# Kernel tuning notes

Hardware: AMD Instinct MI355X
Metric: run time of the kernel (lower is better)

Reference implementation:

```python
import jax, jax.numpy as jnp
import numpy as np

B, N, L, H, K = 65536, 32, 8, 256, 8
RMIN, RMAX = -10.0, 10.0
MIN_BIN, MIN_SLOPE = 1e-4, 1e-4
P = 3 * K + 1  # params per feature per spline


def setup_inputs() -> dict:
    key = jax.random.key(0)
    ks = jax.random.split(key, 20)
    def rn(k, shape, s=0.05):
        return (jax.random.normal(k, shape, dtype=jnp.float32) * s)
    inp = {
        'x': jax.random.normal(ks[0], (B, N), dtype=jnp.float32),
        'sc_scale': 1.0 + rn(ks[1], (L, N)),
        'sc_shift': rn(ks[2], (L, N)),
        'W_in': rn(ks[3], (L, N, H)), 'b_in': rn(ks[4], (L, H)),
        'W1a': rn(ks[5], (L, H, H)), 'b1a': rn(ks[6], (L, H)),
        'W1b': rn(ks[7], (L, H, H)), 'b1b': rn(ks[8], (L, H)),
        'W2a': rn(ks[9], (L, H, H)), 'b2a': rn(ks[10], (L, H)),
        'W2b': rn(ks[11], (L, H, H)), 'b2b': rn(ks[12], (L, H)),
        'W_out': rn(ks[13], (L, H, N * P)), 'b_out': rn(ks[14], (L, N * P)),
        'perms': jnp.asarray(np.stack([np.random.RandomState(i).permutation(N) for i in range(L)]).astype(np.int32)),
    }
    return inp


def _conditioner(mx, Wi, bi, W1a, b1a, W1b, b1b, W2a, b2a, W2b, b2b, Wo, bo):
    # mx: [B, N] masked input -> [B, N, P] spline params
    h = mx @ Wi + bi
    r = jax.nn.relu(jax.nn.relu(h @ W1a + b1a) @ W1b + b1b)
    h = h + r
    r = jax.nn.relu(jax.nn.relu(h @ W2a + b2a) @ W2b + b2b)
    h = h + r
    h = jax.nn.relu(h)
    out = h @ Wo + bo
    return out.reshape(mx.shape[0], N, P)


def _rqs_forward(x, params):
    # x: [B, N]; params: [B, N, 3K+1]. distrax RationalQuadraticSpline forward.
    uw, uh, ud = params[..., :K], params[..., K:2 * K], params[..., 2 * K:]
    total = RMAX - RMIN
    w = jax.nn.softmax(uw, axis=-1) * (total - K * MIN_BIN) + MIN_BIN
    hgt = jax.nn.softmax(uh, axis=-1) * (total - K * MIN_BIN) + MIN_BIN
    zpad = jnp.zeros_like(w[..., :1])
    xp = RMIN + jnp.concatenate([zpad, jnp.cumsum(w, -1)], -1)   # [B,N,K+1]
    yp = RMIN + jnp.concatenate([zpad, jnp.cumsum(hgt, -1)], -1)
    offset = float(np.log(np.expm1(1.0 - MIN_SLOPE)))
    d = jax.nn.softplus(ud + offset) + MIN_SLOPE                  # [B,N,K+1]
    inside = (x > RMIN) & (x < RMAX)
    xc = jnp.clip(x, RMIN, RMAX)
    # per-element bin search (knot positions vary per element)
    idx = jnp.clip(jnp.sum((xc[..., None] >= xp).astype(jnp.int32), -1) - 1, 0, K - 1)
    g = lambda a, i: jnp.take_along_axis(a, i[..., None], -1)[..., 0]
    xk, xk1 = g(xp, idx), g(xp, idx + 1)
    yk, yk1 = g(yp, idx), g(yp, idx + 1)
    dk, dk1 = g(d, idx), g(d, idx + 1)
    bw = xk1 - xk
    bh = yk1 - yk
    s = bh / bw
    z = jnp.clip((xc - xk) / bw, 0.0, 1.0)
    zz = z * (1.0 - z)
    denom = s + (dk1 + dk - 2.0 * s) * zz
    y = yk + bh * (s * z * z + dk * zz) / denom
    ld = 2.0 * jnp.log(s) + jnp.log(dk1 * z * z + 2.0 * s * zz + dk * (1.0 - z) ** 2) - 2.0 * jnp.log(denom)
    return jnp.where(inside, y, x), jnp.where(inside, ld, 0.0)


def reference(x, sc_scale, sc_shift, W_in, b_in, W1a, b1a, W1b, b1b,
              W2a, b2a, W2b, b2b, W_out, b_out, perms):
    mask0 = (jnp.arange(N) % 2).astype(bool)  # True = identity (masked)
    logdet = jnp.zeros(x.shape[0], dtype=x.dtype)
    for i in range(L):
        # Permute
        x = x[:, perms[i]]
        # Scalar affine on all features (mask_all = all-False coupling)
        x = x * sc_scale[i] + sc_shift[i]
        logdet = logdet + jnp.sum(jnp.log(jnp.abs(sc_scale[i])))
        # RQ-spline masked coupling
        mask = mask0 if i % 2 == 0 else ~mask0
        mx = jnp.where(mask, x, 0.0)
        params = _conditioner(mx, W_in[i], b_in[i], W1a[i], b1a[i], W1b[i], b1b[i],
                              W2a[i], b2a[i], W2b[i], b2b[i], W_out[i], b_out[i])
        y, ld = _rqs_forward(x, params)
        x = jnp.where(mask, x, y)
        logdet = logdet + jnp.sum(jnp.where(mask, 0.0, ld), axis=-1)
    # standard-normal base log prob
    logp = -0.5 * jnp.sum(x * x, axis=-1) - 0.5 * N * float(np.log(2.0 * np.pi))
    return logp + logdet
```

## Files before the change

### kernel.cpp

```cpp
#include <hip/hip_runtime.h>
#include <hip/hip_bf16.h>

typedef __attribute__((ext_vector_type(8))) short bf16x8;
typedef __attribute__((ext_vector_type(16))) float f32x16;
typedef __attribute__((ext_vector_type(2))) float f32x2;

#define DEVFN __device__ __forceinline__

constexpr int NFEAT = 32, NLAYER = 8, HID = 256;
constexpr int HS  = 264;
constexpr int MXS = 40;
constexpr int XS  = 33;
constexpr int WIN_E  = 2 * 256 * 16;
constexpr int WH_E   = 16 * 256 * 16;
constexpr int WOUT_E = 16 * 512 * 16;
constexpr int LAYER_E = WIN_E + 4 * WH_E + WOUT_E;
constexpr size_t WT_BYTES = (size_t)LAYER_E * NLAYER * 2;
constexpr size_t WS_NEEDED = WT_BYTES + NLAYER * 512 * 4 + 4;

constexpr float MIN_BIN = 1e-4f, MIN_SLOPE = 1e-4f;
constexpr float SOFTPLUS_OFF = 0.5411666f;
constexpr float WSCALE = 20.0f - 8.0f * MIN_BIN;

DEVFN unsigned short bf16r(float f) {
    unsigned u = __float_as_uint(f);
    u += 0x7fffu + ((u >> 16) & 1u);
    return (unsigned short)(u >> 16);
}
#if defined(__gfx950__) && __has_builtin(__builtin_amdgcn_cvt_pk_bf16_f32)
DEVFN unsigned pack2(float a, float b) {
    auto r = __builtin_amdgcn_cvt_pk_bf16_f32(a, b);
    return __builtin_bit_cast(unsigned, r);
}
#else
DEVFN unsigned pack2(float a, float b) {
    return (unsigned)bf16r(a) | ((unsigned)bf16r(b) << 16);
}
#endif
DEVFN float bflo(unsigned v) { return __uint_as_float(v << 16); }
DEVFN float bfhi(unsigned v) { return __uint_as_float(v & 0xffff0000u); }
DEVFN float frcp(float x) { return __builtin_amdgcn_rcpf(x); }
DEVFN f32x2 vmax0(f32x2 v) {
// ... 38 lines not shown
            dst[o] = (short)bf16r(lb[kk * 256 + n]);
        }
    } else if (b < 656) {
        int id = b - 528; int l = id >> 4, ks = id & 15; int par = l & 1;
        const float* src = Wout + (size_t)l * 256 * 800 + ks * 16 * 800;
        for (int k = 0; k < 16; k++)
            for (int c = t; c < 800; c += 256) lb[k * 800 + c] = src[k * 800 + c];
        __syncthreads();
        short* dst = wt + (size_t)l * LAYER_E + WIN_E + 4 * WH_E + ks * 8192;
#pragma unroll
        for (int i = 0; i < 32; i++) {
            int o = t + i * 256; int c = o >> 4, kk = o & 15;
            int u = c >> 5, p = c & 31;
            float v = (p < 25) ? lb[kk * 800 + (2 * u + par) * 25 + p] : 0.0f;
            dst[o] = (short)bf16r(v);
        }
    } else {
#pragma unroll
        for (int i = 0; i < 16; i++) {
            int idx = t + i * 256;
            int l = idx >> 9, c = idx & 511, u = c >> 5, p = c & 31;
            bo_t[idx] = (p < 25) ? bout[l * 800 + (2 * u + (l & 1)) * 25 + p] : 0.0f;
        }
        lb[t] = logf(fabsf(scS[t]));
        __syncthreads();
        for (int s = 128; s > 0; s >>= 1) { if (t < s) lb[t] += lb[t + s]; __syncthreads(); }
        if (t == 0) *sld = lb[0];
    }
}

template<int KSTEPS, int NSUB, int DEPTH>
DEVFN void gemm_flip(const short* __restrict__ wt, int ntot, int nbase,
                     const unsigned short* __restrict__ B, int bs,
                     f32x16 (&acc)[NSUB][2])
{
    constexpr int D = (KSTEPS < DEPTH) ? KSTEPS : DEPTH;
    const int lane = threadIdx.x & 63;
    const int l31 = lane & 31, l5 = lane >> 5;
    const bf16x8* __restrict__ w8 = (const bf16x8*)wt;
    const int wb = (nbase + l31) * 2 + l5;
    const int krow = ntot * 2;
    bf16x8 a[D][NSUB];
#pragma unroll
    for (int p = 0; p < D; p++)
#pragma unroll
        for (int s = 0; s < NSUB; s++) a[p][s] = w8[(size_t)p * krow + wb + s * 64];
    const unsigned short* bp = B + l31 * bs + l5 * 8;
#pragma unroll
    for (int k = 0; k < KSTEPS; k++) {
        bf16x8 b0 = *(const bf16x8*)(bp + k * 16);
        bf16x8 b1 = *(const bf16x8*)(bp + 32 * bs + k * 16);
#pragma unroll
        for (int s = 0; s < NSUB; s++) {
            acc[s][0] = __builtin_amdgcn_mfma_f32_32x32x16_bf16(a[k % D][s], b0, acc[s][0], 0, 0, 0);
            acc[s][1] = __builtin_amdgcn_mfma_f32_32x32x16_bf16(a[k % D][s], b1, acc[s][1], 0, 0, 0);
        }
        if (k + D < KSTEPS) {
#pragma unroll
            for (int s = 0; s < NSUB; s++) a[k % D][s] = w8[(size_t)(k + D) * krow + wb + s * 64];
        }
    }
}

DEVFN void binit(f32x16& a, const float* __restrict__ bias)
{
    const int q = (threadIdx.x >> 5) & 1;
    const float* bp = bias + 4 * q;
#pragma unroll
    for (int g = 0; g < 4; g++) {
        float4 b = *(const float4*)(bp + 8 * g);
        a[4*g+0] = b.x; a[4*g+1] = b.y; a[4*g+2] = b.z; a[4*g+3] = b.w;
    }
}

template<int MODE>
DEVFN void store_h(const f32x16& v, unsigned short* buf, int m0, int n0)
{
    const int lane = threadIdx.x & 63;
    const int m = m0 + (lane & 31);
    const int q = lane >> 5;
    unsigned short* rowp = buf + m * HS + n0 + 4 * q;
#pragma unroll
    for (int g = 0; g < 4; g++) {
        f32x2 r0 = {v[4*g+0], v[4*g+1]};
        f32x2 r1 = {v[4*g+2], v[4*g+3]};
        if (MODE >= 1) { r0 = vmax0(r0); r1 = vmax0(r1); }
        unsigned short* dst = rowp + 8 * g;
        if (MODE >= 2) {
            uint2 old = *(const uint2*)dst;
            r0 += (f32x2){bflo(old.x), bfhi(old.x)};
            r1 += (f32x2){bflo(old.y), bfhi(old.y)};
            if (MODE == 3) { r0 = vmax0(r0); r1 = vmax0(r1); }
        }
        uint2 pk;
        pk.x = pack2(r0.x, r0.y);
        pk.y = pack2(r1.x, r1.y);
        *(uint2*)dst = pk;
    }
}

__global__ __launch_bounds__(256, 2) void flow_kernel(
    const float* __restrict__ x_in, const float* __restrict__ scS, const float* __restrict__ scB,
    const float* __restrict__ bin, const float* __restrict__ b1a, const float* __restrict__ b1b,
    const float* __restrict__ b2a, const float* __restrict__ b2b,
    const int* __restrict__ perms,
    const short* __restrict__ wt, const float* __restrict__ bo_t, const float* __restrict__ sld,
    float* __restrict__ out)
{
    __shared__ __align__(16) unsigned short hS[64 * HS];
    __shared__ __align__(16) unsigned short uS[64 * HS];
    __shared__ float xS[64 * XS];
    __shared__ float redS[256];

    const int tid = threadIdx.x;
    const int wave = tid >> 6;
    const int lane = tid & 63;
    const int q = lane >> 5;
    const size_t rowbase = (size_t)blockIdx.x * 64;
    unsigned short* tS  = uS;
    unsigned short* mxS = uS;

#pragma unroll
    for (int i = 0; i < 8; i++) {
        int g = tid + i * 256;
        xS[(g >> 5) * XS + (g & 31)] = x_in[rowbase * NFEAT + g];
    }
    float ld_acc = 0.0f;
    __syncthreads();

    const int nbase = wave * 64;

#pragma unroll 1
    for (int l = 0; l < NLAYER; l++) {
        const int par = l & 1;
        const short* wb = wt + (size_t)l * LAYER_E;

        {
            int j = tid & 31; int r0 = (tid >> 5) * 8;
            int pj = perms[l * 32 + j];
            float sc = scS[l * 32 + j], sh = scB[l * 32 + j];
            float vals[8];
#pragma unroll
            for (int r = 0; r < 8; r++) vals[r] = xS[(r0 + r) * XS + pj] * sc + sh;
            __syncthreads();
            int keep = ((j & 1) != par);
#pragma unroll
            for (int r = 0; r < 8; r++) {
                xS[(r0 + r) * XS + j] = vals[r];
                mxS[(r0 + r) * MXS + j] = keep ? bf16r(vals[r]) : (unsigned short)0;
            }
            __syncthreads();
        }
        {
            f32x16 acc[2][2];
            binit(acc[0][0], bin + l * 256 + nbase);      binit(acc[0][1], bin + l * 256 + nbase);
            binit(acc[1][0], bin + l * 256 + nbase + 32); binit(acc[1][1], bin + l * 256 + nbase + 32);
            gemm_flip<2, 2, 2>(wb, 256, nbase, mxS, MXS, acc);
#pragma unroll
            for (int s = 0; s < 2; s++) {
                store_h<0>(acc[s][0], hS, 0,  nbase + s * 32);
                store_h<0>(acc[s][1], hS, 32, nbase + s * 32);
            }
            __syncthreads();
        }
        {
            f32x16 acc[2][2];
            binit(acc[0][0], b1a + l * 256 + nbase);      binit(acc[0][1], b1a + l * 256 + nbase);
            binit(acc[1][0], b1a + l * 256 + nbase + 32); binit(acc[1][1], b1a + l * 256 + nbase + 32);
            gemm_flip<16, 2, 4>(wb + WIN_E, 256, nbase, hS, HS, acc);
#pragma unroll
            for (int s = 0; s < 2; s++) {
                store_h<1>(acc[s][0], tS, 0,  nbase + s * 32);
                store_h<1>(acc[s][1], tS, 32, nbase + s * 32);
            }
            __syncthreads();
        }
        {
            f32x16 acc[2][2];
            binit(acc[0][0], b1b + l * 256 + nbase);      binit(acc[0][1], b1b + l * 256 + nbase);
            binit(acc[1][0], b1b + l * 256 + nbase + 32); binit(acc[1][1], b1b + l * 256 + nbase + 32);
            gemm_flip<16, 2, 4>(wb + WIN_E + WH_E, 256, nbase, tS, HS, acc);
#pragma unroll
            for (int s = 0; s < 2; s++) {
                store_h<2>(acc[s][0], hS, 0,  nbase + s * 32);
                store_h<2>(acc[s][1], hS, 32, nbase + s * 32);
            }
            __syncthreads();
        }
        {
            f32x16 acc[2][2];
            binit(acc[0][0], b2a + l * 256 + nbase);      binit(acc[0][1], b2a + l * 256 + nbase);
            binit(acc[1][0], b2a + l * 256 + nbase + 32); binit(acc[1][1], b2a + l * 256 + nbase + 32);
            gemm_flip<16, 2, 4>(wb + WIN_E + 2 * WH_E, 256, nbase, hS, HS, acc);
#pragma unroll
            for (int s = 0; s < 2; s++) {
                store_h<1>(acc[s][0], tS, 0,  nbase + s * 32);
                store_h<1>(acc[s][1], tS, 32, nbase + s * 32);
            }
            __syncthreads();
        }
        {
            f32x16 acc[2][2];
            binit(acc[0][0], b2b + l * 256 + nbase);      binit(acc[0][1], b2b + l * 256 + nbase);
            binit(acc[1][0], b2b + l * 256 + nbase + 32); binit(acc[1][1], b2b + l * 256 + nbase + 32);
            gemm_flip<16, 2, 4>(wb + WIN_E + 3 * WH_E, 256, nbase, tS, HS, acc);
#pragma unroll
            for (int s = 0; s < 2; s++) {
                store_h<3>(acc[s][0], hS, 0,  nbase + s * 32);
                store_h<3>(acc[s][1], hS, 32, nbase + s * 32);
            }
            __syncthreads();
        }
        {
            const short* wo = wb + WIN_E + 4 * WH_E;
            f32x16 acc[4][2];
            const float* bb = bo_t + l * 512 + wave * 128;
#pragma unroll
            for (int s = 0; s < 4; s++) { binit(acc[s][0], bb + s * 32); binit(acc[s][1], bb + s * 32); }
            gemm_flip<16, 4, 2>(wo, 512, wave * 128, hS, HS, acc);

#pragma unroll
            for (int s = 0; s < 4; s++) {
                float exch[16];
#pragma unroll
                for (int i = 0; i < 16; i++) {
                    float snd = q ? acc[s][0][i] : acc[s][1][i];
                    exch[i] = __shfl_xor(snd, 32, 64);
                }
                float A0[16], A1[16];
#pragma unroll
                for (int i = 0; i < 16; i++) {
                    float kept = q ? acc[s][1][i] : acc[s][0][i];
                    A0[i] = q ? exch[i] : kept;
                    A1[i] = q ? kept : exch[i];
                }
                float P[25];
#pragma unroll
                for (int p = 0; p < 25; p++) {
                    int rg = (p & 3) + 4 * (p >> 3);
                    P[p] = ((p >> 2) & 1) ? A1[rg] : A0[rg];
                }
                int n = 2 * (4 * wave + s) + par;
                float xv = xS[lane * XS + n];
                float ew[8], eh[8], sw = 0.f, sh2 = 0.f;
#pragma unroll
                for (int i = 0; i < 8; i++) { ew[i] = __expf(P[i]); sw += ew[i]; }
#pragma unroll
                for (int i = 0; i < 8; i++) { eh[i] = __expf(P[8 + i]); sh2 += eh[i]; }
                float fw = WSCALE * frcp(sw), fh = WSCALE * frcp(sh2);
                float w[8], hh[8];
#pragma unroll
                for (int i = 0; i < 8; i++) { w[i] = fmaf(ew[i], fw, MIN_BIN); hh[i] = fmaf(eh[i], fh, MIN_BIN); }

                bool inside = (xv > -10.0f) && (xv < 10.0f);
                float xc = fminf(fmaxf(xv, -10.0f), 10.0f);
                float cx = -10.0f + w[0], cy = -10.0f + hh[0];
                float xk = -10.0f, yk = -10.0f, bw = w[0], bh = hh[0];
                float udk = P[16], udk1 = P[17];
#pragma unroll
                for (int i = 1; i < 8; i++) {
                    bool take = (xc >= cx);
                    if (take) { xk = cx; yk = cy; bw = w[i]; bh = hh[i]; udk = P[16 + i]; udk1 = P[17 + i]; }
                    cx += w[i]; cy += hh[i];
                }
                float dk  = __logf(1.f + __expf(udk  + SOFTPLUS_OFF)) + MIN_SLOPE;
                float dk1 = __logf(1.f + __expf(udk1 + SOFTPLUS_OFF)) + MIN_SLOPE;
                float ibw = frcp(bw);
                float s_ = bh * ibw;
                float z = fminf(fmaxf((xc - xk) * ibw, 0.0f), 1.0f);
                float omz = 1.0f - z;
                float zz = z * omz;
                float denom = fmaf(dk1 + dk - 2.0f * s_, zz, s_);
                float idenom = frcp(denom);
                float y = fmaf(bh * fmaf(s_ * z, z, dk * zz), idenom, yk);
                float num = fmaf(dk1 * z, z, fmaf(2.0f * s_, zz, dk * omz * omz));
                float ldv = 2.0f * __logf(s_ * idenom) + __logf(num);
                xS[lane * XS + n] = inside ? y : xv;
                ld_acc += inside ? ldv : 0.0f;
            }
            __syncthreads();
        }
    }
    {
        int m = tid & 63, jg = tid >> 6;
        float s2 = 0.f;
#pragma unroll
        for (int j = 0; j < 8; j++) { float v = xS[m * XS + jg * 8 + j]; s2 += v * v; }
        redS[tid] = ld_acc - 0.5f * s2;
        __syncthreads();
        if (tid < 64) {
            float tot = redS[tid] + redS[tid + 64] + redS[tid + 128] + redS[tid + 192]
                      + *sld - 29.406033062549525f;
            out[rowbase + tid] = tot;
        }
    }
}

extern "C" void kernel_launch(void* const* d_in, const int* in_sizes, int n_in,
                              void* d_out, int out_size, void* d_ws, size_t ws_size,
                              hipStream_t stream) {
    if (ws_size < WS_NEEDED) return;
    const float* x    = (const float*)d_in[0];
    const float* scS  = (const float*)d_in[1];
    const float* scB  = (const float*)d_in[2];
    const float* Win  = (const float*)d_in[3];
    const float* bin  = (const float*)d_in[4];
    const float* W1a  = (const float*)d_in[5];
    const float* b1a  = (const float*)d_in[6];
    const float* W1b  = (const float*)d_in[7];
    const float* b1b  = (const float*)d_in[8];
    const float* W2a  = (const float*)d_in[9];
    const float* b2a  = (const float*)d_in[10];
    const float* W2b  = (const float*)d_in[11];
    const float* b2b  = (const float*)d_in[12];
    const float* Wout = (const float*)d_in[13];
    const float* bout = (const float*)d_in[14];
    const int* perms  = (const int*)d_in[15];

    short* wt   = (short*)d_ws;
    float* bo_t = (float*)((char*)d_ws + WT_BYTES);
    float* sld  = bo_t + NLAYER * 512;

    prep_kernel<<<657, 256, 0, stream>>>(Win, W1a, W1b, W2a, W2b, Wout, bout, scS, wt, bo_t, sld);
    flow_kernel<<<65536 / 64, 256, 0, stream>>>(x, scS, scB, bin, b1a, b1b, b2a, b2b,
                                                perms, wt, bo_t, sld, (float*)d_out);
}
```

Baseline: 573.9 us.

## Split each 64-row block across eight waves instead of four

Doubles the block to 512 threads so each wave computes 32 hidden columns (and 64 output columns) instead of 64/128. All GEMM stages, the spline epilogue, the x-permute stage and the final reduction are re-indexed for eight waves. The aim is more waves per CU and fewer accumulator registers per wave, which helps latency hiding. The cost is that each wave reuses every loaded activation fragment over fewer columns, so LDS reads per MFMA go up, and the barriers now cover more waves.

```diff
diff --git a/kernel.cpp b/kernel.cpp
--- a/kernel.cpp
+++ b/kernel.cpp
@@ -179,7 +179,7 @@
     }
 }
 
-__global__ __launch_bounds__(256, 2) void flow_kernel(
+__global__ __launch_bounds__(512, 4) void flow_kernel(
     const float* __restrict__ x_in, const float* __restrict__ scS, const float* __restrict__ scB,
     const float* __restrict__ bin, const float* __restrict__ b1a, const float* __restrict__ b1b,
     const float* __restrict__ b2a, const float* __restrict__ b2b,
@@ -190,7 +190,7 @@
     __shared__ __align__(16) unsigned short hS[64 * HS];
     __shared__ __align__(16) unsigned short uS[64 * HS];
     __shared__ float xS[64 * XS];
-    __shared__ float redS[256];
+    __shared__ float redS[512];
 
     const int tid = threadIdx.x;
     const int wave = tid >> 6;
@@ -201,14 +201,14 @@
     unsigned short* mxS = uS;
 
 #pragma unroll
-    for (int i = 0; i < 8; i++) {
-        int g = tid + i * 256;
+    for (int i = 0; i < 4; i++) {
+        int g = tid + i * 512;
         xS[(g >> 5) * XS + (g & 31)] = x_in[rowbase * NFEAT + g];
     }
     float ld_acc = 0.0f;
     __syncthreads();
 
-    const int nbase = wave * 64;
+    const int nbase = wave * 32;
 
 #pragma unroll 1
     for (int l = 0; l < NLAYER; l++) {
@@ -216,91 +216,76 @@
         const short* wb = wt + (size_t)l * LAYER_E;
 
         {
-            int j = tid & 31; int r0 = (tid >> 5) * 8;
+            int j = tid & 31; int r0 = (tid >> 5) * 4;
             int pj = perms[l * 32 + j];
             float sc = scS[l * 32 + j], sh = scB[l * 32 + j];
-            float vals[8];
-#pragma unroll
-            for (int r = 0; r < 8; r++) vals[r] = xS[(r0 + r) * XS + pj] * sc + sh;
+            float vals[4];
+#pragma unroll
+            for (int r = 0; r < 4; r++) vals[r] = xS[(r0 + r) * XS + pj] * sc + sh;
             __syncthreads();
             int keep = ((j & 1) != par);
 #pragma unroll
-            for (int r = 0; r < 8; r++) {
+            for (int r = 0; r < 4; r++) {
                 xS[(r0 + r) * XS + j] = vals[r];
                 mxS[(r0 + r) * MXS + j] = keep ? bf16r(vals[r]) : (unsigned short)0;
             }
             __syncthreads();
         }
         {
+            f32x16 acc[1][2];
+            binit(acc[0][0], bin + l * 256 + nbase);
+            binit(acc[0][1], bin + l * 256 + nbase);
+            gemm_flip<2, 1, 2>(wb, 256, nbase, mxS, MXS, acc);
+            store_h<0>(acc[0][0], hS, 0,  nbase);
+            store_h<0>(acc[0][1], hS, 32, nbase);
+            __syncthreads();
+        }
+        {
+            f32x16 acc[1][2];
+            binit(acc[0][0], b1a + l * 256 + nbase);
+            binit(acc[0][1], b1a + l * 256 + nbase);
+            gemm_flip<16, 1, 4>(wb + WIN_E, 256, nbase, hS, HS, acc);
+            store_h<1>(acc[0][0], tS, 0,  nbase);
+            store_h<1>(acc[0][1], tS, 32, nbase);
+            __syncthreads();
+        }
+        {
+            f32x16 acc[1][2];
+            binit(acc[0][0], b1b + l * 256 + nbase);
+            binit(acc[0][1], b1b + l * 256 + nbase);
+            gemm_flip<16, 1, 4>(wb + WIN_E + WH_E, 256, nbase, tS, HS, acc);
+            store_h<2>(acc[0][0], hS, 0,  nbase);
+            store_h<2>(acc[0][1], hS, 32, nbase);
+            __syncthreads();
+        }
+        {
+            f32x16 acc[1][2];
+            binit(acc[0][0], b2a + l * 256 + nbase);
+            binit(acc[0][1], b2a + l * 256 + nbase);
+            gemm_flip<16, 1, 4>(wb + WIN_E + 2 * WH_E, 256, nbase, hS, HS, acc);
+            store_h<1>(acc[0][0], tS, 0,  nbase);
+            store_h<1>(acc[0][1], tS, 32, nbase);
+            __syncthreads();
+        }
+        {
+            f32x16 acc[1][2];
+            binit(acc[0][0], b2b + l * 256 + nbase);
+            binit(acc[0][1], b2b + l * 256 + nbase);
+            gemm_flip<16, 1, 4>(wb + WIN_E + 3 * WH_E, 256, nbase, tS, HS, acc);
+            store_h<3>(acc[0][0], hS, 0,  nbase);
+            store_h<3>(acc[0][1], hS, 32, nbase);
+            __syncthreads();
+        }
+        {
+            const short* wo = wb + WIN_E + 4 * WH_E;
             f32x16 acc[2][2];
-            binit(acc[0][0], bin + l * 256 + nbase);      binit(acc[0][1], bin + l * 256 + nbase);
-            binit(acc[1][0], bin + l * 256 + nbase + 32); binit(acc[1][1], bin + l * 256 + nbase + 32);
-            gemm_flip<2, 2, 2>(wb, 256, nbase, mxS, MXS, acc);
+            const float* bb = bo_t + l * 512 + wave * 64;
+#pragma unroll
+            for (int s = 0; s < 2; s++) { binit(acc[s][0], bb + s * 32); binit(acc[s][1], bb + s * 32); }
+            gemm_flip<16, 2, 2>(wo, 512, wave * 64, hS, HS, acc);
+
 #pragma unroll
             for (int s = 0; s < 2; s++) {
-                store_h<0>(acc[s][0], hS, 0,  nbase + s * 32);
-                store_h<0>(acc[s][1], hS, 32, nbase + s * 32);
-            }
-            __syncthreads();
-        }
-        {
-            f32x16 acc[2][2];
-            binit(acc[0][0], b1a + l * 256 + nbase);      binit(acc[0][1], b1a + l * 256 + nbase);
-            binit(acc[1][0], b1a + l * 256 + nbase + 32); binit(acc[1][1], b1a + l * 256 + nbase + 32);
-            gemm_flip<16, 2, 4>(wb + WIN_E, 256, nbase, hS, HS, acc);
-#pragma unroll
-            for (int s = 0; s < 2; s++) {
-                store_h<1>(acc[s][0], tS, 0,  nbase + s * 32);
-                store_h<1>(acc[s][1], tS, 32, nbase + s * 32);
-            }
-            __syncthreads();
-        }
-        {
-            f32x16 acc[2][2];
-            binit(acc[0][0], b1b + l * 256 + nbase);      binit(acc[0][1], b1b + l * 256 + nbase);
-            binit(acc[1][0], b1b + l * 256 + nbase + 32); binit(acc[1][1], b1b + l * 256 + nbase + 32);
-            gemm_flip<16, 2, 4>(wb + WIN_E + WH_E, 256, nbase, tS, HS, acc);
-#pragma unroll
-            for (int s = 0; s < 2; s++) {
-                store_h<2>(acc[s][0], hS, 0,  nbase + s * 32);
-                store_h<2>(acc[s][1], hS, 32, nbase + s * 32);
-            }
-            __syncthreads();
-        }
-        {
-            f32x16 acc[2][2];
-            binit(acc[0][0], b2a + l * 256 + nbase);      binit(acc[0][1], b2a + l * 256 + nbase);
-            binit(acc[1][0], b2a + l * 256 + nbase + 32); binit(acc[1][1], b2a + l * 256 + nbase + 32);
-            gemm_flip<16, 2, 4>(wb + WIN_E + 2 * WH_E, 256, nbase, hS, HS, acc);
-#pragma unroll
-            for (int s = 0; s < 2; s++) {
-                store_h<1>(acc[s][0], tS, 0,  nbase + s * 32);
-                store_h<1>(acc[s][1], tS, 32, nbase + s * 32);
-            }
-            __syncthreads();
-        }
-        {
-            f32x16 acc[2][2];
-            binit(acc[0][0], b2b + l * 256 + nbase);      binit(acc[0][1], b2b + l * 256 + nbase);
-            binit(acc[1][0], b2b + l * 256 + nbase + 32); binit(acc[1][1], b2b + l * 256 + nbase + 32);
-            gemm_flip<16, 2, 4>(wb + WIN_E + 3 * WH_E, 256, nbase, tS, HS, acc);
-#pragma unroll
-            for (int s = 0; s < 2; s++) {
-                store_h<3>(acc[s][0], hS, 0,  nbase + s * 32);
-                store_h<3>(acc[s][1], hS, 32, nbase + s * 32);
-            }
-            __syncthreads();
-        }
-        {
-            const short* wo = wb + WIN_E + 4 * WH_E;
-            f32x16 acc[4][2];
-            const float* bb = bo_t + l * 512 + wave * 128;
-#pragma unroll
-            for (int s = 0; s < 4; s++) { binit(acc[s][0], bb + s * 32); binit(acc[s][1], bb + s * 32); }
-            gemm_flip<16, 4, 2>(wo, 512, wave * 128, hS, HS, acc);
-
-#pragma unroll
-            for (int s = 0; s < 4; s++) {
                 float exch[16];
 #pragma unroll
                 for (int i = 0; i < 16; i++) {
@@ -320,7 +305,7 @@
                     int rg = (p & 3) + 4 * (p >> 3);
                     P[p] = ((p >> 2) & 1) ? A1[rg] : A0[rg];
                 }
-                int n = 2 * (4 * wave + s) + par;
+                int n = 2 * (2 * wave + s) + par;
                 float xv = xS[lane * XS + n];
                 float ew[8], eh[8], sw = 0.f, sh2 = 0.f;
 #pragma unroll
@@ -365,12 +350,13 @@
         int m = tid & 63, jg = tid >> 6;
         float s2 = 0.f;
 #pragma unroll
-        for (int j = 0; j < 8; j++) { float v = xS[m * XS + jg * 8 + j]; s2 += v * v; }
+        for (int j = 0; j < 4; j++) { float v = xS[m * XS + jg * 4 + j]; s2 += v * v; }
         redS[tid] = ld_acc - 0.5f * s2;
         __syncthreads();
         if (tid < 64) {
-            float tot = redS[tid] + redS[tid + 64] + redS[tid + 128] + redS[tid + 192]
-                      + *sld - 29.406033062549525f;
+            float tot = *sld - 29.406033062549525f;
+#pragma unroll
+            for (int g = 0; g < 8; g++) tot += redS[tid + 64 * g];
             out[rowbase + tid] = tot;
         }
     }
@@ -402,6 +388,6 @@
     float* sld  = bo_t + NLAYER * 512;
 
     prep_kernel<<<657, 256, 0, stream>>>(Win, W1a, W1b, W2a, W2b, Wout, bout, scS, wt, bo_t, sld);
-    flow_kernel<<<65536 / 64, 256, 0, stream>>>(x, scS, scB, bin, b1a, b1b, b2a, b2b,
+    flow_kernel<<<65536 / 64, 512, 0, stream>>>(x, scS, scB, bin, b1a, b1b, b2a, b2b,
                                                 perms, wt, bo_t, sld, (float*)d_out);
 }
```

Result: slower. 694.3 us (+21.0%).

## Shrink flow block to 32 rows with two waves spanning wider column tiles

Applied to the files above, without the earlier changes.

The fused flow kernel now runs 128-thread blocks that each process 32 batch rows instead of 256-thread blocks of 64 rows. Each wave now computes 128 output columns with four MFMA subtiles against a single 32-row B tile. The output projection is split into two passes so register use stays bounded. This roughly halves LDS per block and doubles the block count, aiming for higher occupancy, but each global weight fragment is now reused for only one MFMA instead of two, which doubles weight traffic per row.

```diff
diff --git a/kernel.cpp b/kernel.cpp
--- a/kernel.cpp
+++ b/kernel.cpp
@@ -8,6 +8,7 @@
 #define DEVFN __device__ __forceinline__
 
 constexpr int NFEAT = 32, NLAYER = 8, HID = 256;
+constexpr int MROW = 32;
 constexpr int HS  = 264;
 constexpr int MXS = 40;
 constexpr int XS  = 33;
@@ -112,7 +113,7 @@
 template<int KSTEPS, int NSUB, int DEPTH>
 DEVFN void gemm_flip(const short* __restrict__ wt, int ntot, int nbase,
                      const unsigned short* __restrict__ B, int bs,
-                     f32x16 (&acc)[NSUB][2])
+                     f32x16 (&acc)[NSUB])
 {
     constexpr int D = (KSTEPS < DEPTH) ? KSTEPS : DEPTH;
     const int lane = threadIdx.x & 63;
@@ -129,12 +130,9 @@
 #pragma unroll
     for (int k = 0; k < KSTEPS; k++) {
         bf16x8 b0 = *(const bf16x8*)(bp + k * 16);
-        bf16x8 b1 = *(const bf16x8*)(bp + 32 * bs + k * 16);
-#pragma unroll
-        for (int s = 0; s < NSUB; s++) {
-            acc[s][0] = __builtin_amdgcn_mfma_f32_32x32x16_bf16(a[k % D][s], b0, acc[s][0], 0, 0, 0);
-            acc[s][1] = __builtin_amdgcn_mfma_f32_32x32x16_bf16(a[k % D][s], b1, acc[s][1], 0, 0, 0);
-        }
+#pragma unroll
+        for (int s = 0; s < NSUB; s++)
+            acc[s] = __builtin_amdgcn_mfma_f32_32x32x16_bf16(a[k % D][s], b0, acc[s], 0, 0, 0);
         if (k + D < KSTEPS) {
 #pragma unroll
             for (int s = 0; s < NSUB; s++) a[k % D][s] = w8[(size_t)(k + D) * krow + wb + s * 64];
@@ -154,10 +152,10 @@
 }
 
 template<int MODE>
-DEVFN void store_h(const f32x16& v, unsigned short* buf, int m0, int n0)
+DEVFN void store_h(const f32x16& v, unsigned short* buf, int n0)
 {
     const int lane = threadIdx.x & 63;
-    const int m = m0 + (lane & 31);
+    const int m = lane & 31;
     const int q = lane >> 5;
     unsigned short* rowp = buf + m * HS + n0 + 4 * q;
 #pragma unroll
@@ -179,7 +177,7 @@
     }
 }
 
-__global__ __launch_bounds__(256, 2) void flow_kernel(
+__global__ __launch_bounds__(128, 2) void flow_kernel(
     const float* __restrict__ x_in, const float* __restrict__ scS, const float* __restrict__ scB,
     const float* __restrict__ bin, const float* __restrict__ b1a, const float* __restrict__ b1b,
     const float* __restrict__ b2a, const float* __restrict__ b2b,
@@ -187,28 +185,28 @@
     const short* __restrict__ wt, const float* __restrict__ bo_t, const float* __restrict__ sld,
     float* __restrict__ out)
 {
-    __shared__ __align__(16) unsigned short hS[64 * HS];
-    __shared__ __align__(16) unsigned short uS[64 * HS];
-    __shared__ float xS[64 * XS];
-    __shared__ float redS[256];
+    __shared__ __align__(16) unsigned short hS[MROW * HS];
+    __shared__ __align__(16) unsigned short uS[MROW * HS];
+    __shared__ float xS[MROW * XS];
+    __shared__ float redS[128];
 
     const int tid = threadIdx.x;
     const int wave = tid >> 6;
     const int lane = tid & 63;
     const int q = lane >> 5;
-    const size_t rowbase = (size_t)blockIdx.x * 64;
+    const size_t rowbase = (size_t)blockIdx.x * MROW;
     unsigned short* tS  = uS;
     unsigned short* mxS = uS;
 
 #pragma unroll
     for (int i = 0; i < 8; i++) {
-        int g = tid + i * 256;
+        int g = tid + i * 128;
         xS[(g >> 5) * XS + (g & 31)] = x_in[rowbase * NFEAT + g];
     }
     float ld_acc = 0.0f;
     __syncthreads();
 
-    const int nbase = wave * 64;
+    const int nbase = wave * 128;
 
 #pragma unroll 1
     for (int l = 0; l < NLAYER; l++) {
@@ -232,144 +230,134 @@
             __syncthreads();
         }
         {
-            f32x16 acc[2][2];
-            binit(acc[0][0], bin + l * 256 + nbase);      binit(acc[0][1], bin + l * 256 + nbase);
-            binit(acc[1][0], bin + l * 256 + nbase + 32); binit(acc[1][1], bin + l * 256 + nbase + 32);
-            gemm_flip<2, 2, 2>(wb, 256, nbase, mxS, MXS, acc);
-#pragma unroll
-            for (int s = 0; s < 2; s++) {
-                store_h<0>(acc[s][0], hS, 0,  nbase + s * 32);
-                store_h<0>(acc[s][1], hS, 32, nbase + s * 32);
+            f32x16 acc[4];
+#pragma unroll
+            for (int s = 0; s < 4; s++) binit(acc[s], bin + l * 256 + nbase + s * 32);
+            gemm_flip<2, 4, 2>(wb, 256, nbase, mxS, MXS, acc);
+#pragma unroll
+            for (int s = 0; s < 4; s++) store_h<0>(acc[s], hS, nbase + s * 32);
+            __syncthreads();
+        }
+        {
+            f32x16 acc[4];
+#pragma unroll
+            for (int s = 0; s < 4; s++) binit(acc[s], b1a + l * 256 + nbase + s * 32);
+            gemm_flip<16, 4, 3>(wb + WIN_E, 256, nbase, hS, HS, acc);
+#pragma unroll
+            for (int s = 0; s < 4; s++) store_h<1>(acc[s], tS, nbase + s * 32);
+            __syncthreads();
+        }
+        {
+            f32x16 acc[4];
+#pragma unroll
+            for (int s = 0; s < 4; s++) binit(acc[s], b1b + l * 256 + nbase + s * 32);
+            gemm_flip<16, 4, 3>(wb + WIN_E + WH_E, 256, nbase, tS, HS, acc);
+#pragma unroll
+            for (int s = 0; s < 4; s++) store_h<2>(acc[s], hS, nbase + s * 32);
+            __syncthreads();
+        }
+        {
+            f32x16 acc[4];
+#pragma unroll
+            for (int s = 0; s < 4; s++) binit(acc[s], b2a + l * 256 + nbase + s * 32);
+            gemm_flip<16, 4, 3>(wb + WIN_E + 2 * WH_E, 256, nbase, hS, HS, acc);
+#pragma unroll
+            for (int s = 0; s < 4; s++) store_h<1>(acc[s], tS, nbase + s * 32);
+            __syncthreads();
+        }
+        {
+            f32x16 acc[4];
+#pragma unroll
+            for (int s = 0; s < 4; s++) binit(acc[s], b2b + l * 256 + nbase + s * 32);
+            gemm_flip<16, 4, 3>(wb + WIN_E + 3 * WH_E, 256, nbase, tS, HS, acc);
+#pragma unroll
+            for (int s = 0; s < 4; s++) store_h<3>(acc[s], hS, nbase + s * 32);
+            __syncthreads();
+        }
+        {
+            const short* wo = wb + WIN_E + 4 * WH_E;
+#pragma unroll 1
+            for (int pass = 0; pass < 2; pass++) {
+                f32x16 acc[4];
+                const float* bb = bo_t + l * 512 + pass * 256 + wave * 128;
+#pragma unroll
+                for (int s = 0; s < 4; s++) binit(acc[s], bb + s * 32);
+                gemm_flip<16, 4, 2>(wo, 512, pass * 256 + wave * 128, hS, HS, acc);
+
+#pragma unroll
+                for (int pr = 0; pr < 2; pr++) {
+                    const int sa = 2 * pr, sb = sa + 1;
+                    float exch[16];
+#pragma unroll
+                    for (int i = 0; i < 16; i++) {
+                        float snd = q ? acc[sa][i] : acc[sb][i];
+                        exch[i] = __shfl_xor(snd, 32, 64);
+                    }
+                    float A0[16], A1[16];
+#pragma unroll
+                    for (int i = 0; i < 16; i++) {
+                        A0[i] = q ? exch[i] : acc[sa][i];
+                        A1[i] = q ? acc[sb][i] : exch[i];
+                    }
+                    float P[25];
+#pragma unroll
+                    for (int p = 0; p < 25; p++) {
+                        int rg = (p & 3) + 4 * (p >> 3);
+                        P[p] = ((p >> 2) & 1) ? A1[rg] : A0[rg];
+                    }
+                    int u = pass * 8 + wave * 4 + (q ? sb : sa);
+                    int n = 2 * u + par;
+                    int m = lane & 31;
+                    float xv = xS[m * XS + n];
+                    float ew[8], eh[8], sw = 0.f, sh2 = 0.f;
+#pragma unroll
+                    for (int i = 0; i < 8; i++) { ew[i] = __expf(P[i]); sw += ew[i]; }
+#pragma unroll
+                    for (int i = 0; i < 8; i++) { eh[i] = __expf(P[8 + i]); sh2 += eh[i]; }
+                    float fw = WSCALE * frcp(sw), fh = WSCALE * frcp(sh2);
+                    float w[8], hh[8];
+#pragma unroll
+                    for (int i = 0; i < 8; i++) { w[i] = fmaf(ew[i], fw, MIN_BIN); hh[i] = fmaf(eh[i], fh, MIN_BIN); }
+
+                    bool inside = (xv > -10.0f) && (xv < 10.0f);
+                    float xc = fminf(fmaxf(xv, -10.0f), 10.0f);
+                    float cx = -10.0f + w[0], cy = -10.0f + hh[0];
+                    float xk = -10.0f, yk = -10.0f, bw = w[0], bh = hh[0];
+                    float udk = P[16], udk1 = P[17];
+#pragma unroll
+                    for (int i = 1; i < 8; i++) {
+                        bool take = (xc >= cx);
+                        if (take) { xk = cx; yk = cy; bw = w[i]; bh = hh[i]; udk = P[16 + i]; udk1 = P[17 + i]; }
+                        cx += w[i]; cy += hh[i];
+                    }
+                    float dk  = __logf(1.f + __expf(udk  + SOFTPLUS_OFF)) + MIN_SLOPE;
+                    float dk1 = __logf(1.f + __expf(udk1 + SOFTPLUS_OFF)) + MIN_SLOPE;
+                    float ibw = frcp(bw);
+                    float s_ = bh * ibw;
+                    float z = fminf(fmaxf((xc - xk) * ibw, 0.0f), 1.0f);
+                    float omz = 1.0f - z;
+                    float zz = z * omz;
+                    float denom = fmaf(dk1 + dk - 2.0f * s_, zz, s_);
+                    float idenom = frcp(denom);
+                    float y = fmaf(bh * fmaf(s_ * z, z, dk * zz), idenom, yk);
+                    float num = fmaf(dk1 * z, z, fmaf(2.0f * s_, zz, dk * omz * omz));
+                    float ldv = 2.0f * __logf(s_ * idenom) + __logf(num);
+                    xS[m * XS + n] = inside ? y : xv;
+                    ld_acc += inside ? ldv : 0.0f;
+                }
             }
             __syncthreads();
         }
-        {
-            f32x16 acc[2][2];
-            binit(acc[0][0], b1a + l * 256 + nbase);      binit(acc[0][1], b1a + l * 256 + nbase);
-            binit(acc[1][0], b1a + l * 256 + nbase + 32); binit(acc[1][1], b1a + l * 256 + nbase + 32);
-            gemm_flip<16, 2, 4>(wb + WIN_E, 256, nbase, hS, HS, acc);
-#pragma unroll
-            for (int s = 0; s < 2; s++) {
-                store_h<1>(acc[s][0], tS, 0,  nbase + s * 32);
-                store_h<1>(acc[s][1], tS, 32, nbase + s * 32);
-            }
-            __syncthreads();
-        }
-        {
-            f32x16 acc[2][2];
-            binit(acc[0][0], b1b + l * 256 + nbase);      binit(acc[0][1], b1b + l * 256 + nbase);
-            binit(acc[1][0], b1b + l * 256 + nbase + 32); binit(acc[1][1], b1b + l * 256 + nbase + 32);
-            gemm_flip<16, 2, 4>(wb + WIN_E + WH_E, 256, nbase, tS, HS, acc);
-#pragma unroll
-            for (int s = 0; s < 2; s++) {
-                store_h<2>(acc[s][0], hS, 0,  nbase + s * 32);
-                store_h<2>(acc[s][1], hS, 32, nbase + s * 32);
-            }
-            __syncthreads();
-        }
-        {
-            f32x16 acc[2][2];
-            binit(acc[0][0], b2a + l * 256 + nbase);      binit(acc[0][1], b2a + l * 256 + nbase);
-            binit(acc[1][0], b2a + l * 256 + nbase + 32); binit(acc[1][1], b2a + l * 256 + nbase + 32);
-            gemm_flip<16, 2, 4>(wb + WIN_E + 2 * WH_E, 256, nbase, hS, HS, acc);
-#pragma unroll
-            for (int s = 0; s < 2; s++) {
-                store_h<1>(acc[s][0], tS, 0,  nbase + s * 32);
-                store_h<1>(acc[s][1], tS, 32, nbase + s * 32);
-            }
-            __syncthreads();
-        }
-        {
-            f32x16 acc[2][2];
-            binit(acc[0][0], b2b + l * 256 + nbase);      binit(acc[0][1], b2b + l * 256 + nbase);
-            binit(acc[1][0], b2b + l * 256 + nbase + 32); binit(acc[1][1], b2b + l * 256 + nbase + 32);
-            gemm_flip<16, 2, 4>(wb + WIN_E + 3 * WH_E, 256, nbase, tS, HS, acc);
-#pragma unroll
-            for (int s = 0; s < 2; s++) {
-                store_h<3>(acc[s][0], hS, 0,  nbase + s * 32);
-                store_h<3>(acc[s][1], hS, 32, nbase + s * 32);
-            }
-            __syncthreads();
-        }
-        {
-            const short* wo = wb + WIN_E + 4 * WH_E;
-            f32x16 acc[4][2];
-            const float* bb = bo_t + l * 512 + wave * 128;
-#pragma unroll
-            for (int s = 0; s < 4; s++) { binit(acc[s][0], bb + s * 32); binit(acc[s][1], bb + s * 32); }
-            gemm_flip<16, 4, 2>(wo, 512, wave * 128, hS, HS, acc);
-
-#pragma unroll
-            for (int s = 0; s < 4; s++) {
-                float exch[16];
-#pragma unroll
-                for (int i = 0; i < 16; i++) {
-                    float snd = q ? acc[s][0][i] : acc[s][1][i];
-                    exch[i] = __shfl_xor(snd, 32, 64);
-                }
-                float A0[16], A1[16];
-#pragma unroll
-                for (int i = 0; i < 16; i++) {
-                    float kept = q ? acc[s][1][i] : acc[s][0][i];
-                    A0[i] = q ? exch[i] : kept;
-                    A1[i] = q ? kept : exch[i];
-                }
-                float P[25];
-#pragma unroll
-                for (int p = 0; p < 25; p++) {
-                    int rg = (p & 3) + 4 * (p >> 3);
-                    P[p] = ((p >> 2) & 1) ? A1[rg] : A0[rg];
-                }
-                int n = 2 * (4 * wave + s) + par;
-                float xv = xS[lane * XS + n];
-                float ew[8], eh[8], sw = 0.f, sh2 = 0.f;
-#pragma unroll
-                for (int i = 0; i < 8; i++) { ew[i] = __expf(P[i]); sw += ew[i]; }
-#pragma unroll
-                for (int i = 0; i < 8; i++) { eh[i] = __expf(P[8 + i]); sh2 += eh[i]; }
-                float fw = WSCALE * frcp(sw), fh = WSCALE * frcp(sh2);
-                float w[8], hh[8];
-#pragma unroll
-                for (int i = 0; i < 8; i++) { w[i] = fmaf(ew[i], fw, MIN_BIN); hh[i] = fmaf(eh[i], fh, MIN_BIN); }
-
-                bool inside = (xv > -10.0f) && (xv < 10.0f);
-                float xc = fminf(fmaxf(xv, -10.0f), 10.0f);
-                float cx = -10.0f + w[0], cy = -10.0f + hh[0];
-                float xk = -10.0f, yk = -10.0f, bw = w[0], bh = hh[0];
-                float udk = P[16], udk1 = P[17];
-#pragma unroll
-                for (int i = 1; i < 8; i++) {
-                    bool take = (xc >= cx);
-                    if (take) { xk = cx; yk = cy; bw = w[i]; bh = hh[i]; udk = P[16 + i]; udk1 = P[17 + i]; }
-                    cx += w[i]; cy += hh[i];
-                }
-                float dk  = __logf(1.f + __expf(udk  + SOFTPLUS_OFF)) + MIN_SLOPE;
-                float dk1 = __logf(1.f + __expf(udk1 + SOFTPLUS_OFF)) + MIN_SLOPE;
-                float ibw = frcp(bw);
-                float s_ = bh * ibw;
-                float z = fminf(fmaxf((xc - xk) * ibw, 0.0f), 1.0f);
-                float omz = 1.0f - z;
-                float zz = z * omz;
-                float denom = fmaf(dk1 + dk - 2.0f * s_, zz, s_);
-                float idenom = frcp(denom);
-                float y = fmaf(bh * fmaf(s_ * z, z, dk * zz), idenom, yk);
-                float num = fmaf(dk1 * z, z, fmaf(2.0f * s_, zz, dk * omz * omz));
-                float ldv = 2.0f * __logf(s_ * idenom) + __logf(num);
-                xS[lane * XS + n] = inside ? y : xv;
-                ld_acc += inside ? ldv : 0.0f;
-            }
-            __syncthreads();
-        }
     }
     {
-        int m = tid & 63, jg = tid >> 6;
+        int m = tid & 31, jg = tid >> 5;
         float s2 = 0.f;
 #pragma unroll
         for (int j = 0; j < 8; j++) { float v = xS[m * XS + jg * 8 + j]; s2 += v * v; }
         redS[tid] = ld_acc - 0.5f * s2;
         __syncthreads();
-        if (tid < 64) {
-            float tot = redS[tid] + redS[tid + 64] + redS[tid + 128] + redS[tid + 192]
+        if (tid < 32) {
+            float tot = redS[tid] + redS[tid + 32] + redS[tid + 64] + redS[tid + 96]
                       + *sld - 29.406033062549525f;
             out[rowbase + tid] = tot;
         }
@@ -402,6 +390,6 @@
     float* sld  = bo_t + NLAYER * 512;
 
     prep_kernel<<<657, 256, 0, stream>>>(Win, W1a, W1b, W2a, W2b, Wout, bout, scS, wt, bo_t, sld);
-    flow_kernel<<<65536 / 64, 256, 0, stream>>>(x, scS, scB, bin, b1a, b1b, b2a, b2b,
-                                                perms, wt, bo_t, sld, (float*)d_out);
-}
+    flow_kernel<<<65536 / MROW, 128, 0, stream>>>(x, scS, scB, bin, b1a, b1b, b2a, b2b,
+                                                  perms, wt, bo_t, sld, (float*)d_out);
+}
```

Measured after the change: 1.183 ms. 106% more time.

## Merge two 64-row groups per block with staggered phase schedule

Applied to the files above, without the earlier changes.

Each block now holds two independent 64-row groups of 4 waves. The layer loop is flattened into 8 phases per layer, and the second group runs 4 phases behind the first. The aim is for one group's GEMM phases to overlap the other group's spline or permute phases, so MFMA and VALU work mix within a CU. The cost is that a block-wide barrier now follows every phase, so the two groups sync together, and occupancy shifts from two 256-thread blocks to one 512-thread block per CU.

```diff
diff --git a/kernel.cpp b/kernel.cpp
--- a/kernel.cpp
+++ b/kernel.cpp
@@ -179,7 +179,7 @@
     }
 }
 
-__global__ __launch_bounds__(256, 2) void flow_kernel(
+__global__ __launch_bounds__(512, 1) void flow_kernel(
     const float* __restrict__ x_in, const float* __restrict__ scS, const float* __restrict__ scB,
     const float* __restrict__ bin, const float* __restrict__ b1a, const float* __restrict__ b1b,
     const float* __restrict__ b2a, const float* __restrict__ b2b,
@@ -187,191 +187,200 @@
     const short* __restrict__ wt, const float* __restrict__ bo_t, const float* __restrict__ sld,
     float* __restrict__ out)
 {
-    __shared__ __align__(16) unsigned short hS[64 * HS];
-    __shared__ __align__(16) unsigned short uS[64 * HS];
-    __shared__ float xS[64 * XS];
-    __shared__ float redS[256];
-
-    const int tid = threadIdx.x;
+    __shared__ __align__(16) unsigned short hSS[2][64 * HS];
+    __shared__ __align__(16) unsigned short uSS[2][64 * HS];
+    __shared__ float xSS[2][64 * XS];
+    __shared__ float redS[512];
+
+    const int tid  = threadIdx.x;
     const int wave = tid >> 6;
+    const int grp  = wave >> 2;
+    const int gw   = wave & 3;
     const int lane = tid & 63;
-    const int q = lane >> 5;
-    const size_t rowbase = (size_t)blockIdx.x * 64;
-    unsigned short* tS  = uS;
-    unsigned short* mxS = uS;
+    const int q    = lane >> 5;
+    const int gtid = tid & 255;
+
+    const size_t rowbase = (size_t)blockIdx.x * 128 + (size_t)grp * 64;
+    unsigned short* hG = hSS[grp];
+    unsigned short* uG = uSS[grp];
+    float* xG = xSS[grp];
 
 #pragma unroll
     for (int i = 0; i < 8; i++) {
-        int g = tid + i * 256;
-        xS[(g >> 5) * XS + (g & 31)] = x_in[rowbase * NFEAT + g];
+        int g = gtid + i * 256;
+        xG[(g >> 5) * XS + (g & 31)] = x_in[rowbase * NFEAT + g];
     }
     float ld_acc = 0.0f;
     __syncthreads();
 
-    const int nbase = wave * 64;
+    const int nbase = gw * 64;
+    float pvals[8];
+
+    constexpr int PH = 8, TOT = NLAYER * PH, OFF = 4;
 
 #pragma unroll 1
-    for (int l = 0; l < NLAYER; l++) {
-        const int par = l & 1;
-        const short* wb = wt + (size_t)l * LAYER_E;
-
-        {
-            int j = tid & 31; int r0 = (tid >> 5) * 8;
-            int pj = perms[l * 32 + j];
-            float sc = scS[l * 32 + j], sh = scB[l * 32 + j];
-            float vals[8];
-#pragma unroll
-            for (int r = 0; r < 8; r++) vals[r] = xS[(r0 + r) * XS + pj] * sc + sh;
-            __syncthreads();
-            int keep = ((j & 1) != par);
-#pragma unroll
-            for (int r = 0; r < 8; r++) {
-                xS[(r0 + r) * XS + j] = vals[r];
-                mxS[(r0 + r) * MXS + j] = keep ? bf16r(vals[r]) : (unsigned short)0;
+    for (int seg = 0; seg < TOT + OFF; ++seg) {
+        int p = seg - (grp ? OFF : 0);
+        if (p >= 0 && p < TOT) {
+            const int l = p >> 3, ph = p & 7;
+            const int par = l & 1;
+            const short* wb = wt + (size_t)l * LAYER_E;
+            switch (ph) {
+            case 0: {
+                int j = gtid & 31; int r0 = (gtid >> 5) * 8;
+                int pj = perms[l * 32 + j];
+                float sc = scS[l * 32 + j], sh = scB[l * 32 + j];
+#pragma unroll
+                for (int r = 0; r < 8; r++) pvals[r] = xG[(r0 + r) * XS + pj] * sc + sh;
+            } break;
+            case 1: {
+                int j = gtid & 31; int r0 = (gtid >> 5) * 8;
+                int keep = ((j & 1) != par);
+#pragma unroll
+                for (int r = 0; r < 8; r++) {
+                    xG[(r0 + r) * XS + j] = pvals[r];
+                    uG[(r0 + r) * MXS + j] = keep ? bf16r(pvals[r]) : (unsigned short)0;
+                }
+            } break;
+            case 2: {
+                f32x16 acc[2][2];
+                binit(acc[0][0], bin + l * 256 + nbase);      binit(acc[0][1], bin + l * 256 + nbase);
+                binit(acc[1][0], bin + l * 256 + nbase + 32); binit(acc[1][1], bin + l * 256 + nbase + 32);
+                gemm_flip<2, 2, 2>(wb, 256, nbase, uG, MXS, acc);
+#pragma unroll
+                for (int s = 0; s < 2; s++) {
+                    store_h<0>(acc[s][0], hG, 0,  nbase + s * 32);
+                    store_h<0>(acc[s][1], hG, 32, nbase + s * 32);
+                }
+            } break;
+            case 3: {
+                f32x16 acc[2][2];
+                binit(acc[0][0], b1a + l * 256 + nbase);      binit(acc[0][1], b1a + l * 256 + nbase);
+                binit(acc[1][0], b1a + l * 256 + nbase + 32); binit(acc[1][1], b1a + l * 256 + nbase + 32);
+                gemm_flip<16, 2, 4>(wb + WIN_E, 256, nbase, hG, HS, acc);
+#pragma unroll
+                for (int s = 0; s < 2; s++) {
+                    store_h<1>(acc[s][0], uG, 0,  nbase + s * 32);
+                    store_h<1>(acc[s][1], uG, 32, nbase + s * 32);
+                }
+            } break;
+            case 4: {
+                f32x16 acc[2][2];
+                binit(acc[0][0], b1b + l * 256 + nbase);      binit(acc[0][1], b1b + l * 256 + nbase);
+                binit(acc[1][0], b1b + l * 256 + nbase + 32); binit(acc[1][1], b1b + l * 256 + nbase + 32);
+                gemm_flip<16, 2, 4>(wb + WIN_E + WH_E, 256, nbase, uG, HS, acc);
+#pragma unroll
+                for (int s = 0; s < 2; s++) {
+                    store_h<2>(acc[s][0], hG, 0,  nbase + s * 32);
+                    store_h<2>(acc[s][1], hG, 32, nbase + s * 32);
+                }
+            } break;
+            case 5: {
+                f32x16 acc[2][2];
+                binit(acc[0][0], b2a + l * 256 + nbase);      binit(acc[0][1], b2a + l * 256 + nbase);
+                binit(acc[1][0], b2a + l * 256 + nbase + 32); binit(acc[1][1], b2a + l * 256 + nbase + 32);
+                gemm_flip<16, 2, 4>(wb + WIN_E + 2 * WH_E, 256, nbase, hG, HS, acc);
+#pragma unroll
+                for (int s = 0; s < 2; s++) {
+                    store_h<1>(acc[s][0], uG, 0,  nbase + s * 32);
+                    store_h<1>(acc[s][1], uG, 32, nbase + s * 32);
+                }
+            } break;
+            case 6: {
+                f32x16 acc[2][2];
+                binit(acc[0][0], b2b + l * 256 + nbase);      binit(acc[0][1], b2b + l * 256 + nbase);
+                binit(acc[1][0], b2b + l * 256 + nbase + 32); binit(acc[1][1], b2b + l * 256 + nbase + 32);
+                gemm_flip<16, 2, 4>(wb + WIN_E + 3 * WH_E, 256, nbase, uG, HS, acc);
+#pragma unroll
+                for (int s = 0; s < 2; s++) {
+                    store_h<3>(acc[s][0], hG, 0,  nbase + s * 32);
+                    store_h<3>(acc[s][1], hG, 32, nbase + s * 32);
+                }
+            } break;
+            default: {
+                const short* wo = wb + WIN_E + 4 * WH_E;
+                f32x16 acc[4][2];
+                const float* bb = bo_t + l * 512 + gw * 128;
+#pragma unroll
+                for (int s = 0; s < 4; s++) { binit(acc[s][0], bb + s * 32); binit(acc[s][1], bb + s * 32); }
+                gemm_flip<16, 4, 2>(wo, 512, gw * 128, hG, HS, acc);
+
+#pragma unroll
+                for (int s = 0; s < 4; s++) {
+                    float exch[16];
+#pragma unroll
+                    for (int i = 0; i < 16; i++) {
+                        float snd = q ? acc[s][0][i] : acc[s][1][i];
+                        exch[i] = __shfl_xor(snd, 32, 64);
+                    }
+                    float A0[16], A1[16];
+#pragma unroll
+                    for (int i = 0; i < 16; i++) {
+                        float kept = q ? acc[s][1][i] : acc[s][0][i];
+                        A0[i] = q ? exch[i] : kept;
+                        A1[i] = q ? kept : exch[i];
+                    }
+                    float P[25];
+#pragma unroll
+                    for (int pi = 0; pi < 25; pi++) {
+                        int rg = (pi & 3) + 4 * (pi >> 3);
+                        P[pi] = ((pi >> 2) & 1) ? A1[rg] : A0[rg];
+                    }
+                    int n = 2 * (4 * gw + s) + par;
+                    float xv = xG[lane * XS + n];
+                    float ew[8], eh[8], sw = 0.f, sh2 = 0.f;
+#pragma unroll
+                    for (int i = 0; i < 8; i++) { ew[i] = __expf(P[i]); sw += ew[i]; }
+#pragma unroll
+                    for (int i = 0; i < 8; i++) { eh[i] = __expf(P[8 + i]); sh2 += eh[i]; }
+                    float fw = WSCALE * frcp(sw), fh = WSCALE * frcp(sh2);
+                    float w[8], hh[8];
+#pragma unroll
+                    for (int i = 0; i < 8; i++) { w[i] = fmaf(ew[i], fw, MIN_BIN); hh[i] = fmaf(eh[i], fh, MIN_BIN); }
+
+                    bool inside = (xv > -10.0f) && (xv < 10.0f);
+                    float xc = fminf(fmaxf(xv, -10.0f), 10.0f);
+                    float cx = -10.0f + w[0], cy = -10.0f + hh[0];
+                    float xk = -10.0f, yk = -10.0f, bw = w[0], bh = hh[0];
+                    float udk = P[16], udk1 = P[17];
+#pragma unroll
+                    for (int i = 1; i < 8; i++) {
+                        bool take = (xc >= cx);
+                        if (take) { xk = cx; yk = cy; bw = w[i]; bh = hh[i]; udk = P[16 + i]; udk1 = P[17 + i]; }
+                        cx += w[i]; cy += hh[i];
+                    }
+                    float dk  = __logf(1.f + __expf(udk  + SOFTPLUS_OFF)) + MIN_SLOPE;
+                    float dk1 = __logf(1.f + __expf(udk1 + SOFTPLUS_OFF)) + MIN_SLOPE;
+                    float ibw = frcp(bw);
+                    float s_ = bh * ibw;
+                    float z = fminf(fmaxf((xc - xk) * ibw, 0.0f), 1.0f);
+                    float omz = 1.0f - z;
+                    float zz = z * omz;
+                    float denom = fmaf(dk1 + dk - 2.0f * s_, zz, s_);
+                    float idenom = frcp(denom);
+                    float y = fmaf(bh * fmaf(s_ * z, z, dk * zz), idenom, yk);
+                    float num = fmaf(dk1 * z, z, fmaf(2.0f * s_, zz, dk * omz * omz));
+                    float ldv = 2.0f * __logf(s_ * idenom) + __logf(num);
+                    xG[lane * XS + n] = inside ? y : xv;
+                    ld_acc += inside ? ldv : 0.0f;
+                }
+            } break;
             }
-            __syncthreads();
-        }
-        {
-            f32x16 acc[2][2];
-            binit(acc[0][0], bin + l * 256 + nbase);      binit(acc[0][1], bin + l * 256 + nbase);
-            binit(acc[1][0], bin + l * 256 + nbase + 32); binit(acc[1][1], bin + l * 256 + nbase + 32);
-            gemm_flip<2, 2, 2>(wb, 256, nbase, mxS, MXS, acc);
-#pragma unroll
-            for (int s = 0; s < 2; s++) {
-                store_h<0>(acc[s][0], hS, 0,  nbase + s * 32);
-                store_h<0>(acc[s][1], hS, 32, nbase + s * 32);
-            }
-            __syncthreads();
-        }
-        {
-            f32x16 acc[2][2];
-            binit(acc[0][0], b1a + l * 256 + nbase);      binit(acc[0][1], b1a + l * 256 + nbase);
-            binit(acc[1][0], b1a + l * 256 + nbase + 32); binit(acc[1][1], b1a + l * 256 + nbase + 32);
-            gemm_flip<16, 2, 4>(wb + WIN_E, 256, nbase, hS, HS, acc);
-#pragma unroll
-            for (int s = 0; s < 2; s++) {
-                store_h<1>(acc[s][0], tS, 0,  nbase + s * 32);
-                store_h<1>(acc[s][1], tS, 32, nbase + s * 32);
-            }
-            __syncthreads();
-        }
-        {
-            f32x16 acc[2][2];
-            binit(acc[0][0], b1b + l * 256 + nbase);      binit(acc[0][1], b1b + l * 256 + nbase);
-            binit(acc[1][0], b1b + l * 256 + nbase + 32); binit(acc[1][1], b1b + l * 256 + nbase + 32);
-            gemm_flip<16, 2, 4>(wb + WIN_E + WH_E, 256, nbase, tS, HS, acc);
-#pragma unroll
-            for (int s = 0; s < 2; s++) {
-                store_h<2>(acc[s][0], hS, 0,  nbase + s * 32);
-                store_h<2>(acc[s][1], hS, 32, nbase + s * 32);
-            }
-            __syncthreads();
-        }
-        {
-            f32x16 acc[2][2];
-            binit(acc[0][0], b2a + l * 256 + nbase);      binit(acc[0][1], b2a + l * 256 + nbase);
-            binit(acc[1][0], b2a + l * 256 + nbase + 32); binit(acc[1][1], b2a + l * 256 + nbase + 32);
-            gemm_flip<16, 2, 4>(wb + WIN_E + 2 * WH_E, 256, nbase, hS, HS, acc);
-#pragma unroll
-            for (int s = 0; s < 2; s++) {
-                store_h<1>(acc[s][0], tS, 0,  nbase + s * 32);
-                store_h<1>(acc[s][1], tS, 32, nbase + s * 32);
-            }
-            __syncthreads();
-        }
-        {
-            f32x16 acc[2][2];
-            binit(acc[0][0], b2b + l * 256 + nbase);      binit(acc[0][1], b2b + l * 256 + nbase);
-            binit(acc[1][0], b2b + l * 256 + nbase + 32); binit(acc[1][1], b2b + l * 256 + nbase + 32);
-            gemm_flip<16, 2, 4>(wb + WIN_E + 3 * WH_E, 256, nbase, tS, HS, acc);
-#pragma unroll
-            for (int s = 0; s < 2; s++) {
-                store_h<3>(acc[s][0], hS, 0,  nbase + s * 32);
-                store_h<3>(acc[s][1], hS, 32, nbase + s * 32);
-            }
-            __syncthreads();
-        }
-        {
-            const short* wo = wb + WIN_E + 4 * WH_E;
-            f32x16 acc[4][2];
-            const float* bb = bo_t + l * 512 + wave * 128;
-#pragma unroll
-            for (int s = 0; s < 4; s++) { binit(acc[s][0], bb + s * 32); binit(acc[s][1], bb + s * 32); }
-            gemm_flip<16, 4, 2>(wo, 512, wave * 128, hS, HS, acc);
-
-#pragma unroll
-            for (int s = 0; s < 4; s++) {
-                float exch[16];
-#pragma unroll
-                for (int i = 0; i < 16; i++) {
-                    float snd = q ? acc[s][0][i] : acc[s][1][i];
-                    exch[i] = __shfl_xor(snd, 32, 64);
-                }
-                float A0[16], A1[16];
-#pragma unroll
-                for (int i = 0; i < 16; i++) {
-                    float kept = q ? acc[s][1][i] : acc[s][0][i];
-                    A0[i] = q ? exch[i] : kept;
-                    A1[i] = q ? kept : exch[i];
-                }
-                float P[25];
-#pragma unroll
-                for (int p = 0; p < 25; p++) {
-                    int rg = (p & 3) + 4 * (p >> 3);
-                    P[p] = ((p >> 2) & 1) ? A1[rg] : A0[rg];
-                }
-                int n = 2 * (4 * wave + s) + par;
-                float xv = xS[lane * XS + n];
-                float ew[8], eh[8], sw = 0.f, sh2 = 0.f;
-#pragma unroll
-                for (int i = 0; i < 8; i++) { ew[i] = __expf(P[i]); sw += ew[i]; }
-#pragma unroll
-                for (int i = 0; i < 8; i++) { eh[i] = __expf(P[8 + i]); sh2 += eh[i]; }
-                float fw = WSCALE * frcp(sw), fh = WSCALE * frcp(sh2);
-                float w[8], hh[8];
-#pragma unroll
-                for (int i = 0; i < 8; i++) { w[i] = fmaf(ew[i], fw, MIN_BIN); hh[i] = fmaf(eh[i], fh, MIN_BIN); }
-
-                bool inside = (xv > -10.0f) && (xv < 10.0f);
-                float xc = fminf(fmaxf(xv, -10.0f), 10.0f);
-                float cx = -10.0f + w[0], cy = -10.0f + hh[0];
-                float xk = -10.0f, yk = -10.0f, bw = w[0], bh = hh[0];
-                float udk = P[16], udk1 = P[17];
-#pragma unroll
-                for (int i = 1; i < 8; i++) {
-                    bool take = (xc >= cx);
-                    if (take) { xk = cx; yk = cy; bw = w[i]; bh = hh[i]; udk = P[16 + i]; udk1 = P[17 + i]; }
-                    cx += w[i]; cy += hh[i];
-                }
-                float dk  = __logf(1.f + __expf(udk  + SOFTPLUS_OFF)) + MIN_SLOPE;
-                float dk1 = __logf(1.f + __expf(udk1 + SOFTPLUS_OFF)) + MIN_SLOPE;
-                float ibw = frcp(bw);
-                float s_ = bh * ibw;
-                float z = fminf(fmaxf((xc - xk) * ibw, 0.0f), 1.0f);
-                float omz = 1.0f - z;
-                float zz = z * omz;
-                float denom = fmaf(dk1 + dk - 2.0f * s_, zz, s_);
-                float idenom = frcp(denom);
-                float y = fmaf(bh * fmaf(s_ * z, z, dk * zz), idenom, yk);
-                float num = fmaf(dk1 * z, z, fmaf(2.0f * s_, zz, dk * omz * omz));
-                float ldv = 2.0f * __logf(s_ * idenom) + __logf(num);
-                xS[lane * XS + n] = inside ? y : xv;
-                ld_acc += inside ? ldv : 0.0f;
-            }
-            __syncthreads();
-        }
+        }
+        __syncthreads();
     }
     {
-        int m = tid & 63, jg = tid >> 6;
+        int m = gtid & 63, jg = gtid >> 6;
         float s2 = 0.f;
 #pragma unroll
-        for (int j = 0; j < 8; j++) { float v = xS[m * XS + jg * 8 + j]; s2 += v * v; }
+        for (int j = 0; j < 8; j++) { float v = xG[m * XS + jg * 8 + j]; s2 += v * v; }
         redS[tid] = ld_acc - 0.5f * s2;
         __syncthreads();
-        if (tid < 64) {
-            float tot = redS[tid] + redS[tid + 64] + redS[tid + 128] + redS[tid + 192]
+        if (gtid < 64) {
+            float* rg = redS + grp * 256;
+            float tot = rg[gtid] + rg[gtid + 64] + rg[gtid + 128] + rg[gtid + 192]
                       + *sld - 29.406033062549525f;
-            out[rowbase + tid] = tot;
+            out[rowbase + gtid] = tot;
         }
     }
 }
@@ -402,6 +411,6 @@
     float* sld  = bo_t + NLAYER * 512;
 
     prep_kernel<<<657, 256, 0, stream>>>(Win, W1a, W1b, W2a, W2b, Wout, bout, scS, wt, bo_t, sld);
-    flow_kernel<<<65536 / 64, 256, 0, stream>>>(x, scS, scB, bin, b1a, b1b, b2a, b2b,
-                                                perms, wt, bo_t, sld, (float*)d_out);
-}
+    flow_kernel<<<65536 / 128, 512, 0, stream>>>(x, scS, scB, bin, b1a, b1b, b2a, b2b,
+                                                 perms, wt, bo_t, sld, (float*)d_out);
+}
```

Result: slower. 728.0 us (+26.9%).
